# Kernel optimization log

Measured on AMD Instinct MI355X. Metric: run time of the kernel, lower is better.

Reference implementation:

```python
import jax, jax.numpy as jnp
import numpy as np

B, T, D = 16, 2048, 1024
TT = T - 2            # tokens after stripping BOS/EOS
WORD_EVERY = 3        # a word starts every 3 BPE tokens
MAX_WORDS = TT // WORD_EVERY  # 682
NUM_MUTEX, NUM_BIN = 64, 32


def setup_inputs() -> dict:
    key = jax.random.key(0)
    ks = jax.random.split(key, 7)
    features = jax.random.normal(ks[0], (B, T, D), dtype=jnp.float32)
    word_starts = jnp.zeros((B, TT), dtype=jnp.int32).at[:, ::WORD_EVERY].set(1)
    s = 1.0 / np.sqrt(D)
    dense_w = jax.random.normal(ks[1], (D, D), dtype=jnp.float32) * s
    dense_b = jax.random.normal(ks[2], (D,), dtype=jnp.float32) * 0.01
    out_w = jax.random.normal(ks[3], (NUM_MUTEX, D), dtype=jnp.float32) * s
    out_b = jax.random.normal(ks[4], (NUM_MUTEX,), dtype=jnp.float32) * 0.01
    bin_w = jax.random.normal(ks[5], (NUM_BIN, D + NUM_MUTEX), dtype=jnp.float32) * s
    bin_b = jax.random.normal(ks[6], (NUM_BIN,), dtype=jnp.float32) * 0.01
    return {"features": features, "word_starts": word_starts,
            "dense_w": dense_w, "dense_b": dense_b,
            "out_w": out_w, "out_b": out_b,
            "bin_w": bin_w, "bin_b": bin_b,
            "max_words": MAX_WORDS}


def _word_features(features, word_starts, max_words):
    # strip BOS/EOS
    x = features[:, 1:-1]                                  # [B, TT, D]
    b, tt, d = x.shape
    seg = jnp.cumsum(word_starts, axis=1) - 1              # word id per token; -1 before first start
    valid = seg >= 0
    flat_seg = seg + jnp.arange(b, dtype=seg.dtype)[:, None] * max_words
    overflow = b * max_words                               # dump invalid tokens into extra bucket
    flat_seg = jnp.where(valid, flat_seg, overflow).reshape(-1)
    sums = jax.ops.segment_sum(x.reshape(-1, d), flat_seg,
                               num_segments=b * max_words + 1)[:-1]
    counts = jax.ops.segment_sum(jnp.ones((b * tt,), dtype=x.dtype), flat_seg,
                                 num_segments=b * max_words + 1)[:-1]
    sums = sums.reshape(b, max_words, d)
    counts = counts.reshape(b, max_words, 1)
    # torch code initializes word_features to ONES; empty slots stay 1.0
    return jnp.where(counts > 0, sums, jnp.ones((), dtype=x.dtype))


def reference(features, word_starts, dense_w, dense_b, out_w, out_b, bin_w, bin_b, max_words):
    wf = _word_features(features, word_starts, max_words)   # [B, MW, D]
    # dropout p=0 (eval) -> identity
    h = jnp.tanh(jnp.einsum('bwd,ed->bwe', wf, dense_w) + dense_b)
    word_class_logits = jnp.einsum('bwd,cd->bwc', h, out_w) + out_b
    cat = jnp.concatenate((word_class_logits, h), axis=-1)  # [B, MW, Cm+D]
    binary_logits = jnp.einsum('bwd,cd->bwc', cat, bin_w) + bin_b
    return (word_class_logits, binary_logits)
```

## Files before the change

### kernel.cpp

```cpp
#include <hip/hip_runtime.h>
#include <stdint.h>

#define B_   16
#define T_   2048
#define D_   1024
#define TT_  2046
#define W_   682
#define BW_  (B_ * W_)
#define NMUT 64
#define NBIN 32

#define G_WF   BW_
#define G_DW   1024
#define G_OW   64
#define G_FOLD 32

typedef __attribute__((ext_vector_type(8))) short s8b;
typedef __attribute__((ext_vector_type(4))) float f32x4;

__device__ inline short f2bf(float f) {
    uint32_t u = __builtin_bit_cast(uint32_t, f);
    u += 0x7FFFu + ((u >> 16) & 1u);
    return (short)(u >> 16);
}

__device__ inline float fast_tanh(float x) {
    float xc = fminf(fmaxf(x, -15.f), 15.f);
    float e  = __expf(2.f * xc);
    return 1.f - 2.f / (e + 1.f);
}

__device__ inline void gload_lds16(const void* g, void* l) {
    __builtin_amdgcn_global_load_lds(
        (const __attribute__((address_space(1))) uint32_t*)g,
        (__attribute__((address_space(3))) uint32_t*)l, 16, 0, 0);
}

__global__ __launch_bounds__(256) void k_scan(const int* __restrict__ ws,
                                              int* __restrict__ starts,
                                              int* __restrict__ nwords) {
    __shared__ int wsum[4];
    int b = blockIdx.x;
    int tid = threadIdx.x;
    const int* row = ws + (size_t)b * TT_;
    int vals[8], incl[8];
    int p = 0;
    int t0 = tid * 8;
#pragma unroll
    for (int i = 0; i < 8; ++i) {
        int t = t0 + i;
        int v = (t < TT_) ? row[t] : 0;
        vals[i] = v;
        p += v;
        incl[i] = p;
    }
    int tot = p;
    int lane = tid & 63;
    int x = tot;
#pragma unroll
    for (int off = 1; off < 64; off <<= 1) {
        int v = __shfl_up(x, off);
        if (lane >= off) x += v;
    }
    int wid = tid >> 6;
    if (lane == 63) wsum[wid] = x;
    __syncthreads();
    int wbase = 0;
    for (int q = 0; q < wid; ++q) wbase += wsum[q];
    int excl = wbase + x - tot;
    int* st = starts + (size_t)b * (W_ + 1);
#pragma unroll
    for (int i = 0; i < 8; ++i) {
        if (vals[i]) {
            int w = excl + incl[i] - 1;
            if (w <= W_) st[w] = t0 + i;
        }
    }
    if (tid == 0) {
        int total = wsum[0] + wsum[1] + wsum[2] + wsum[3];
        nwords[b] = total < W_ ? total : W_;
        if (total <= W_) st[total] = TT_;
    }
}

__global__ __launch_bounds__(256) void k_bulk(const float* __restrict__ feat,
                                              const int* __restrict__ starts,
                                              const int* __restrict__ nwords,
                                              const float* __restrict__ dw,
                                              const float* __restrict__ ow,
                                              const float* __restrict__ ob,
                                              const float* __restrict__ bw,
                                              const float* __restrict__ bb,
                                              short* __restrict__ wf,
                                              short* __restrict__ dwb,
                                              short* __restrict__ Bcat,
                                              float* __restrict__ beff) {
    __shared__ float smem[NMUT];
    int blk = blockIdx.x;
    int tid = threadIdx.x;

    if (blk < G_WF) {
        int b = blk / W_;
        int w = blk - b * W_;
        short* outp = wf + (size_t)blk * D_ + tid * 4;
        int nw = nwords[b];
        f32x4 acc = (f32x4){0.f, 0.f, 0.f, 0.f};
        if (w >= nw) {
            acc = (f32x4){1.f, 1.f, 1.f, 1.f};
        } else {
            const int* st = starts + (size_t)b * (W_ + 1);
            int s = st[w], e = st[w + 1];
            const f32x4* base = (const f32x4*)(feat + ((size_t)b * T_ + 1) * D_) + tid;
            for (int t = s; t < e; ++t) {
                f32x4 v = __builtin_nontemporal_load(base + (size_t)t * (D_ / 4));
                acc += v;
            }
        }
        short4 o;
        o.x = f2bf(acc[0]); o.y = f2bf(acc[1]); o.z = f2bf(acc[2]); o.w = f2bf(acc[3]);
        *(short4*)outp = o;
    } else if (blk < G_WF + G_DW) {
        int i = (blk - G_WF) * 256 + tid;
        f32x4 v = __builtin_nontemporal_load((const f32x4*)dw + i);
        short4 o;
        o.x = f2bf(v[0]); o.y = f2bf(v[1]); o.z = f2bf(v[2]); o.w = f2bf(v[3]);
        *(short4*)(dwb + (size_t)i * 4) = o;
    } else if (blk < G_WF + G_DW + G_OW) {
        int i = (blk - (G_WF + G_DW)) * 256 + tid;
        f32x4 v = *((const f32x4*)ow + i);
        short4 o;
        o.x = f2bf(v[0]); o.y = f2bf(v[1]); o.z = f2bf(v[2]); o.w = f2bf(v[3]);
        *(short4*)(Bcat + (size_t)i * 4) = o;
    } else {
        int j = blk - (G_WF + G_DW + G_OW);
        if (tid < NMUT) smem[tid] = bw[(size_t)j * (D_ + NMUT) + tid];
        __syncthreads();
        for (int k = tid; k < D_; k += 256) {
            float acc = bw[(size_t)j * (D_ + NMUT) + NMUT + k];
#pragma unroll 8
            for (int c = 0; c < NMUT; ++c)
                acc = fmaf(smem[c], ow[(size_t)c * D_ + k], acc);
            Bcat[(size_t)(NMUT + j) * D_ + k] = f2bf(acc);
        }
        if (tid == 0) {
            float acc = bb[j];
            for (int c = 0; c < NMUT; ++c) acc = fmaf(smem[c], ob[c], acc);
            beff[j] = acc;
        }
    }
}

__global__ __launch_bounds__(256) void k_gemm1(const short* __restrict__ wf,
                                               const short* __restrict__ dwb,
                                               const float* __restrict__ db,
                                               short* __restrict__ h) {
    __shared__ short As[2][128 * 32];
    __shared__ short Bs[2][128 * 32];
    int tid  = threadIdx.x;
    int lane = tid & 63;
    int w    = tid >> 6;
    int wm = w >> 1, wn = w & 1;
    int bm = blockIdx.x * 128;
    int bn = blockIdx.y * 128;

    int ln = lane & 15;
    int qk = lane >> 4;

    int srow = lane >> 2;
    int scol = (lane & 3) * 8;

    f32x4 acc[4][4];
#pragma unroll
    for (int i = 0; i < 4; ++i)
#pragma unroll
        for (int j = 0; j < 4; ++j) acc[i][j] = (f32x4){0.f, 0.f, 0.f, 0.f};

    for (int kt = 0; kt < D_; kt += 64) {
#pragma unroll
        for (int hh = 0; hh < 2; ++hh) {
#pragma unroll
            for (int p = 0; p < 2; ++p) {
                int chunk = w * 2 + p;
                int arow = bm + chunk * 16 + srow;
                arow = arow < BW_ ? arow : BW_ - 1;
                gload_lds16(wf + (size_t)arow * D_ + kt + hh * 32 + scol,
                            &As[hh][chunk * 512]);
                int brow = bn + chunk * 16 + srow;
                gload_lds16(dwb + (size_t)brow * D_ + kt + hh * 32 + scol,
                            &Bs[hh][chunk * 512]);
            }
        }
        __syncthreads();
#pragma unroll
        for (int hh = 0; hh < 2; ++hh) {
            s8b af[4], bf[4];
#pragma unroll
            for (int i = 0; i < 4; ++i)
                af[i] = *(const s8b*)&As[hh][(wm * 64 + i * 16 + ln) * 32 + qk * 8];
#pragma unroll
            for (int j = 0; j < 4; ++j)
                bf[j] = *(const s8b*)&Bs[hh][(wn * 64 + j * 16 + ln) * 32 + qk * 8];
#pragma unroll
            for (int i = 0; i < 4; ++i)
#pragma unroll
                for (int j = 0; j < 4; ++j)
                    acc[i][j] = __builtin_amdgcn_mfma_f32_16x16x32_bf16(
                        af[i], bf[j], acc[i][j], 0, 0, 0);
        }
        __syncthreads();
    }

    float bias[4];
#pragma unroll
    for (int j = 0; j < 4; ++j) bias[j] = db[bn + wn * 64 + j * 16 + ln];
#pragma unroll
    for (int i = 0; i < 4; ++i) {
        int row0 = bm + wm * 64 + i * 16 + qk * 4;
#pragma unroll
        for (int r = 0; r < 4; ++r) {
            int row = row0 + r;
            if (row < BW_) {
#pragma unroll
                for (int j = 0; j < 4; ++j) {
                    int cn = bn + wn * 64 + j * 16 + ln;
                    h[(size_t)row * D_ + cn] =
                        f2bf(fast_tanh(acc[i][j][r] + bias[j]));
                }
            }
        }
    }
}

__global__ __launch_bounds__(256) void k_gemm2(const short* __restrict__ h,
                                               const short* __restrict__ Bcat,
                                               const float* __restrict__ ob,
                                               const float* __restrict__ beff,
                                               float* __restrict__ out) {
    __shared__ float red[4][6][256];
    int tid  = threadIdx.x;
    int lane = tid & 63;
    int w    = tid >> 6;
    int ln = lane & 15, qk = lane >> 4;
    int m0 = blockIdx.x * 16;

    const short* ap = h    + (size_t)(m0 + ln) * D_ + w * 256 + qk * 8;
    const short* bp = Bcat + (size_t)ln        * D_ + w * 256 + qk * 8;

    f32x4 acc[6];
#pragma unroll
    for (int cj = 0; cj < 6; ++cj) acc[cj] = (f32x4){0.f, 0.f, 0.f, 0.f};

#pragma unroll
    for (int kk = 0; kk < 8; ++kk) {
        s8b af = *(const s8b*)(ap + kk * 32);
#pragma unroll
        for (int cj = 0; cj < 6; ++cj) {
            s8b bf = *(const s8b*)(bp + (size_t)cj * 16 * D_ + kk * 32);
            acc[cj] = __builtin_amdgcn_mfma_f32_16x16x32_bf16(af, bf, acc[cj], 0, 0, 0);
        }
    }

#pragma unroll
    for (int cj = 0; cj < 6; ++cj)
        *(f32x4*)&red[w][cj][lane * 4] = acc[cj];
    __syncthreads();

#pragma unroll
    for (int i = tid; i < 1536; i += 256) {
        int cj = i >> 8;
        int e  = i & 255;
        float v = red[0][cj][e] + red[1][cj][e] + red[2][cj][e] + red[3][cj][e];
        int l = e >> 2, r = e & 3;
        int row = m0 + (l >> 4) * 4 + r;
        int c   = cj * 16 + (l & 15);
        v += (c < NMUT) ? ob[c] : beff[c - NMUT];
        if (c < NMUT) out[(size_t)row * NMUT + c] = v;
        else out[(size_t)BW_ * NMUT + (size_t)row * NBIN + (c - NMUT)] = v;
    }
}

extern "C" void kernel_launch(void* const* d_in, const int* in_sizes, int n_in,
                              void* d_out, int out_size, void* d_ws, size_t ws_size,
                              hipStream_t stream) {
    const float* feat    = (const float*)d_in[0];
    const int*   wstarts = (const int*)d_in[1];
    const float* dw      = (const float*)d_in[2];
    const float* db      = (const float*)d_in[3];
    const float* ow      = (const float*)d_in[4];
    const float* ob      = (const float*)d_in[5];
    const float* bw      = (const float*)d_in[6];
    const float* bb      = (const float*)d_in[7];
    float* out = (float*)d_out;

    char* ws = (char*)d_ws;
    size_t off = 0;
    auto alloc = [&](size_t bytes) {
        void* p = ws + off;
        off += (bytes + 255) & ~(size_t)255;
        return p;
    };
    short* wf     = (short*)alloc((size_t)BW_ * D_ * 2);
    short* h      = (short*)alloc((size_t)BW_ * D_ * 2);
    short* dwb    = (short*)alloc((size_t)D_ * D_ * 2);
    short* Bcat   = (short*)alloc((size_t)(NMUT + NBIN) * D_ * 2);
    float* beff   = (float*)alloc(NBIN * 4);
    int*   starts = (int*)alloc((size_t)B_ * (W_ + 1) * 4);
    int*   nwords = (int*)alloc(B_ * 4);

    k_scan<<<16, 256, 0, stream>>>(wstarts, starts, nwords);
    k_bulk<<<G_WF + G_DW + G_OW + G_FOLD, 256, 0, stream>>>(
        feat, starts, nwords, dw, ow, ob, bw, bb, wf, dwb, Bcat, beff);
    k_gemm1<<<dim3((BW_ + 127) / 128, D_ / 128), 256, 0, stream>>>(wf, dwb, db, h);
    k_gemm2<<<BW_ / 16, 256, 0, stream>>>(h, Bcat, ob, beff, out);
}
```

Baseline: 270.9 us.

## Double-buffer gemm1 K loop with prefetch and N-fastest block order

Restructures the first GEMM's K loop to prefetch the next 32-wide K slice into the alternate LDS buffer while MFMAs run on the current one, replacing the load-all-then-compute pattern with two barriers per 64-K step. It also flattens the grid to 1D with the N tile index varying fastest, so the 8 blocks sharing an A row tile run near each other and reuse it in cache. Global pointers are precomputed once. The single barrier per iteration relies on the async LDS loads completing before the barrier, which adds some risk of a race if the loads are not waited on properly.

```diff
diff --git a/kernel.cpp b/kernel.cpp
--- a/kernel.cpp
+++ b/kernel.cpp
@@ -160,8 +160,10 @@
     int lane = tid & 63;
     int w    = tid >> 6;
     int wm = w >> 1, wn = w & 1;
-    int bm = blockIdx.x * 128;
-    int bn = blockIdx.y * 128;
+
+    int bid = blockIdx.x;
+    int bm = (bid >> 3) * 128;
+    int bn = (bid & 7) * 128;
 
     int ln = lane & 15;
     int qk = lane >> 4;
@@ -169,44 +171,62 @@
     int srow = lane >> 2;
     int scol = (lane & 3) * 8;
 
+    const short* aptr[2];
+    const short* bptr[2];
+    short* adst[2][2];
+    short* bdst[2][2];
+#pragma unroll
+    for (int p = 0; p < 2; ++p) {
+        int chunk = w * 2 + p;
+        int arow = bm + chunk * 16 + srow;
+        arow = arow < BW_ ? arow : BW_ - 1;
+        aptr[p] = wf + (size_t)arow * D_ + scol;
+        int brow = bn + chunk * 16 + srow;
+        bptr[p] = dwb + (size_t)brow * D_ + scol;
+#pragma unroll
+        for (int bufi = 0; bufi < 2; ++bufi) {
+            adst[bufi][p] = &As[bufi][chunk * 512];
+            bdst[bufi][p] = &Bs[bufi][chunk * 512];
+        }
+    }
+
     f32x4 acc[4][4];
 #pragma unroll
     for (int i = 0; i < 4; ++i)
 #pragma unroll
         for (int j = 0; j < 4; ++j) acc[i][j] = (f32x4){0.f, 0.f, 0.f, 0.f};
 
-    for (int kt = 0; kt < D_; kt += 64) {
-#pragma unroll
-        for (int hh = 0; hh < 2; ++hh) {
+#pragma unroll
+    for (int p = 0; p < 2; ++p) {
+        gload_lds16(aptr[p], adst[0][p]);
+        gload_lds16(bptr[p], bdst[0][p]);
+    }
+    __syncthreads();
+
+#pragma unroll 2
+    for (int it = 0; it < 32; ++it) {
+        int cur = it & 1;
+        if (it < 31) {
+            int kn = (it + 1) * 32;
 #pragma unroll
             for (int p = 0; p < 2; ++p) {
-                int chunk = w * 2 + p;
-                int arow = bm + chunk * 16 + srow;
-                arow = arow < BW_ ? arow : BW_ - 1;
-                gload_lds16(wf + (size_t)arow * D_ + kt + hh * 32 + scol,
-                            &As[hh][chunk * 512]);
-                int brow = bn + chunk * 16 + srow;
-                gload_lds16(dwb + (size_t)brow * D_ + kt + hh * 32 + scol,
-                            &Bs[hh][chunk * 512]);
+                gload_lds16(aptr[p] + kn, adst[cur ^ 1][p]);
+                gload_lds16(bptr[p] + kn, bdst[cur ^ 1][p]);
             }
         }
-        __syncthreads();
-#pragma unroll
-        for (int hh = 0; hh < 2; ++hh) {
-            s8b af[4], bf[4];
-#pragma unroll
-            for (int i = 0; i < 4; ++i)
-                af[i] = *(const s8b*)&As[hh][(wm * 64 + i * 16 + ln) * 32 + qk * 8];
+        s8b af[4], bf[4];
+#pragma unroll
+        for (int i = 0; i < 4; ++i)
+            af[i] = *(const s8b*)&As[cur][(wm * 64 + i * 16 + ln) * 32 + qk * 8];
+#pragma unroll
+        for (int j = 0; j < 4; ++j)
+            bf[j] = *(const s8b*)&Bs[cur][(wn * 64 + j * 16 + ln) * 32 + qk * 8];
+#pragma unroll
+        for (int i = 0; i < 4; ++i)
 #pragma unroll
             for (int j = 0; j < 4; ++j)
-                bf[j] = *(const s8b*)&Bs[hh][(wn * 64 + j * 16 + ln) * 32 + qk * 8];
-#pragma unroll
-            for (int i = 0; i < 4; ++i)
-#pragma unroll
-                for (int j = 0; j < 4; ++j)
-                    acc[i][j] = __builtin_amdgcn_mfma_f32_16x16x32_bf16(
-                        af[i], bf[j], acc[i][j], 0, 0, 0);
-        }
+                acc[i][j] = __builtin_amdgcn_mfma_f32_16x16x32_bf16(
+                    af[i], bf[j], acc[i][j], 0, 0, 0);
         __syncthreads();
     }
 
@@ -310,6 +330,6 @@
     k_scan<<<16, 256, 0, stream>>>(wstarts, starts, nwords);
     k_bulk<<<G_WF + G_DW + G_OW + G_FOLD, 256, 0, stream>>>(
         feat, starts, nwords, dw, ow, ob, bw, bb, wf, dwb, Bcat, beff);
-    k_gemm1<<<dim3((BW_ + 127) / 128, D_ / 128), 256, 0, stream>>>(wf, dwb, db, h);
+    k_gemm1<<<688, 256, 0, stream>>>(wf, dwb, db, h);
     k_gemm2<<<BW_ / 16, 256, 0, stream>>>(h, Bcat, ob, beff, out);
 }
```

Result: slower. 276.4 us (+2.0%).

## Load GEMM1 operands directly from global into registers, drop LDS staging

Applied to the files above, without the earlier changes.

The dense GEMM no longer stages A and B tiles through shared memory with global_load_lds and barriers. Each lane now reads its MFMA fragments straight from global memory, relying on L1/L2 for reuse across waves. The grid also becomes 1D, with column tiles varying fastest so adjacent blocks share the same A rows. This removes the barriers and LDS traffic, but gives up explicit data reuse: every wave re-fetches its rows from cache, and the 16-byte strided loads per row may coalesce poorly.

```diff
diff --git a/kernel.cpp b/kernel.cpp
--- a/kernel.cpp
+++ b/kernel.cpp
@@ -28,12 +28,6 @@
     float xc = fminf(fmaxf(x, -15.f), 15.f);
     float e  = __expf(2.f * xc);
     return 1.f - 2.f / (e + 1.f);
-}
-
-__device__ inline void gload_lds16(const void* g, void* l) {
-    __builtin_amdgcn_global_load_lds(
-        (const __attribute__((address_space(1))) uint32_t*)g,
-        (__attribute__((address_space(3))) uint32_t*)l, 16, 0, 0);
 }
 
 __global__ __launch_bounds__(256) void k_scan(const int* __restrict__ ws,
@@ -154,20 +148,29 @@
                                                const short* __restrict__ dwb,
                                                const float* __restrict__ db,
                                                short* __restrict__ h) {
-    __shared__ short As[2][128 * 32];
-    __shared__ short Bs[2][128 * 32];
     int tid  = threadIdx.x;
     int lane = tid & 63;
     int w    = tid >> 6;
     int wm = w >> 1, wn = w & 1;
-    int bm = blockIdx.x * 128;
-    int bn = blockIdx.y * 128;
-
+    int bid = blockIdx.x;
+    int bm = (bid >> 3) * 128;
+    int bn = (bid & 7) * 128;
     int ln = lane & 15;
     int qk = lane >> 4;
 
-    int srow = lane >> 2;
-    int scol = (lane & 3) * 8;
+    const short* ap[4];
+    const short* bp[4];
+#pragma unroll
+    for (int i = 0; i < 4; ++i) {
+        int row = bm + wm * 64 + i * 16 + ln;
+        row = row < BW_ ? row : BW_ - 1;
+        ap[i] = wf + (size_t)row * D_ + qk * 8;
+    }
+#pragma unroll
+    for (int j = 0; j < 4; ++j) {
+        int col = bn + wn * 64 + j * 16 + ln;
+        bp[j] = dwb + (size_t)col * D_ + qk * 8;
+    }
 
     f32x4 acc[4][4];
 #pragma unroll
@@ -175,39 +178,19 @@
 #pragma unroll
         for (int j = 0; j < 4; ++j) acc[i][j] = (f32x4){0.f, 0.f, 0.f, 0.f};
 
-    for (int kt = 0; kt < D_; kt += 64) {
-#pragma unroll
-        for (int hh = 0; hh < 2; ++hh) {
-#pragma unroll
-            for (int p = 0; p < 2; ++p) {
-                int chunk = w * 2 + p;
-                int arow = bm + chunk * 16 + srow;
-                arow = arow < BW_ ? arow : BW_ - 1;
-                gload_lds16(wf + (size_t)arow * D_ + kt + hh * 32 + scol,
-                            &As[hh][chunk * 512]);
-                int brow = bn + chunk * 16 + srow;
-                gload_lds16(dwb + (size_t)brow * D_ + kt + hh * 32 + scol,
-                            &Bs[hh][chunk * 512]);
-            }
-        }
-        __syncthreads();
-#pragma unroll
-        for (int hh = 0; hh < 2; ++hh) {
-            s8b af[4], bf[4];
-#pragma unroll
-            for (int i = 0; i < 4; ++i)
-                af[i] = *(const s8b*)&As[hh][(wm * 64 + i * 16 + ln) * 32 + qk * 8];
+#pragma unroll 4
+    for (int kk = 0; kk < 32; ++kk) {
+        s8b af[4], bf[4];
+#pragma unroll
+        for (int i = 0; i < 4; ++i) af[i] = *(const s8b*)(ap[i] + kk * 32);
+#pragma unroll
+        for (int j = 0; j < 4; ++j) bf[j] = *(const s8b*)(bp[j] + kk * 32);
+#pragma unroll
+        for (int i = 0; i < 4; ++i)
 #pragma unroll
             for (int j = 0; j < 4; ++j)
-                bf[j] = *(const s8b*)&Bs[hh][(wn * 64 + j * 16 + ln) * 32 + qk * 8];
-#pragma unroll
-            for (int i = 0; i < 4; ++i)
-#pragma unroll
-                for (int j = 0; j < 4; ++j)
-                    acc[i][j] = __builtin_amdgcn_mfma_f32_16x16x32_bf16(
-                        af[i], bf[j], acc[i][j], 0, 0, 0);
-        }
-        __syncthreads();
+                acc[i][j] = __builtin_amdgcn_mfma_f32_16x16x32_bf16(
+                    af[i], bf[j], acc[i][j], 0, 0, 0);
     }
 
     float bias[4];
@@ -310,6 +293,6 @@
     k_scan<<<16, 256, 0, stream>>>(wstarts, starts, nwords);
     k_bulk<<<G_WF + G_DW + G_OW + G_FOLD, 256, 0, stream>>>(
         feat, starts, nwords, dw, ow, ob, bw, bb, wf, dwb, Bcat, beff);
-    k_gemm1<<<dim3((BW_ + 127) / 128, D_ / 128), 256, 0, stream>>>(wf, dwb, db, h);
+    k_gemm1<<<688, 256, 0, stream>>>(wf, dwb, db, h);
     k_gemm2<<<BW_ / 16, 256, 0, stream>>>(h, Bcat, ob, beff, out);
 }
```

After: 333.3 us. 23.1% more time.
